# Optimization experiments

Hardware: AMD Instinct MI355X
Metric: run time of the kernel (lower is better)

## Reference

```python
import jax, jax.numpy as jnp
import numpy as np

N = 50000
E = 1600000
IN = 128
HID = 128
OUT = 64
NEG_SLOPE = 0.2  # DGL GATConv default leaky_relu slope


def _gat_layer(h, src, dst, W, al, ar, b, res=None, act=True):
    """DGL GATConv layer on an edge-list graph.
    h: [N, F_in]; W: [F_in, H*D]; al, ar, b: [H, D]; res: None | [N,H,D].
    Returns [N, H, D].
    """
    H, D = al.shape
    f = (h @ W).reshape(N, H, D)                      # fc projection
    el = jnp.sum(f * al, axis=-1)                     # [N, H]
    er = jnp.sum(f * ar, axis=-1)                     # [N, H]
    e = jax.nn.leaky_relu(el[src] + er[dst], NEG_SLOPE)  # [E, H]
    # edge softmax over incoming edges of each dst node
    m = jax.ops.segment_max(e, dst, num_segments=N)   # [N, H]
    ex = jnp.exp(e - m[dst])                          # [E, H]
    s = jax.ops.segment_sum(ex, dst, num_segments=N)  # [N, H]
    alpha = ex / s[dst]                               # [E, H]
    msg = f[src] * alpha[..., None]                   # [E, H, D]
    rst = jax.ops.segment_sum(msg, dst, num_segments=N)  # [N, H, D]
    if res is not None:
        rst = rst + res
    rst = rst + b                                     # bias [H, D] broadcast
    if act:
        rst = jax.nn.elu(rst)
    return rst


def setup_inputs() -> dict:
    key = jax.random.key(0)
    ks = jax.random.split(key, 16)
    x = jax.random.normal(ks[0], (N, IN), dtype=jnp.float32)
    src = jax.random.randint(ks[1], (E,), 0, N)
    dst = jax.random.randint(ks[2], (E,), 0, N)
    sc = 0.05
    # layer 0: IN -> 8 heads x 16, no residual, elu
    W0 = jax.random.normal(ks[3], (IN, 8 * 16), dtype=jnp.float32) * sc
    al0 = jax.random.normal(ks[4], (8, 16), dtype=jnp.float32) * sc
    ar0 = jax.random.normal(ks[5], (8, 16), dtype=jnp.float32) * sc
    b0 = jnp.zeros((8, 16), dtype=jnp.float32)
    # layer 1: HID -> 8 heads x 16, identity residual (HID == 8*16), elu
    W1 = jax.random.normal(ks[6], (HID, 8 * 16), dtype=jnp.float32) * sc
    al1 = jax.random.normal(ks[7], (8, 16), dtype=jnp.float32) * sc
    ar1 = jax.random.normal(ks[8], (8, 16), dtype=jnp.float32) * sc
    b1 = jnp.zeros((8, 16), dtype=jnp.float32)
    # layer 2: HID -> 1 head x 64, linear residual (128 != 64), no act
    W2 = jax.random.normal(ks[9], (HID, 1 * OUT), dtype=jnp.float32) * sc
    al2 = jax.random.normal(ks[10], (1, OUT), dtype=jnp.float32) * sc
    ar2 = jax.random.normal(ks[11], (1, OUT), dtype=jnp.float32) * sc
    b2 = jnp.zeros((1, OUT), dtype=jnp.float32)
    resW2 = jax.random.normal(ks[12], (HID, 1 * OUT), dtype=jnp.float32) * sc
    return {"x": x, "src": src, "dst": dst,
            "W0": W0, "al0": al0, "ar0": ar0, "b0": b0,
            "W1": W1, "al1": al1, "ar1": ar1, "b1": b1,
            "W2": W2, "al2": al2, "ar2": ar2, "b2": b2,
            "resW2": resW2}


def reference(x, src, dst, W0, al0, ar0, b0, W1, al1, ar1, b1,
              W2, al2, ar2, b2, resW2):
    # layer 0: no residual, elu, flatten heads (dropout=0)
    h = _gat_layer(x, src, dst, W0, al0, ar0, b0, res=None, act=True)
    h = h.reshape(N, -1)  # [N, 128]
    # layer 1: identity residual, elu, flatten heads
    res1 = h.reshape(N, 8, 16)
    h = _gat_layer(h, src, dst, W1, al1, ar1, b1, res=res1, act=True)
    h = h.reshape(N, -1)  # [N, 128]
    # layer 2: linear residual, no activation, mean over heads
    res2 = (h @ resW2).reshape(N, 1, OUT)
    h = _gat_layer(h, src, dst, W2, al2, ar2, b2, res=res2, act=False)
    return h.mean(axis=1)  # [N, 64]
```

## Files before the change

kernel.cpp:

```cpp
#include <hip/hip_runtime.h>
#include <hip/hip_fp16.h>
#include <math.h>


#define GN 50000
#define GE 1600000
#define NB 391
#define NBLK_A 512
#define CHUNK 3125

typedef _Float16 half8 __attribute__((ext_vector_type(8)));
typedef _Float16 half4v __attribute__((ext_vector_type(4)));
typedef float f32x4 __attribute__((ext_vector_type(4)));


__global__ __launch_bounds__(256) void bucketA(const int* __restrict__ dst, int* __restrict__ cnt) {
    __shared__ int hist[NB];
    for (int i = threadIdx.x; i < NB; i += 256) hist[i] = 0;
    __syncthreads();
    int b = blockIdx.x;
    int beg = b * CHUNK, end = beg + CHUNK;
    for (int i = beg + threadIdx.x; i < end; i += 256)
        atomicAdd(&hist[dst[i] >> 7], 1);
    __syncthreads();
    for (int k = threadIdx.x; k < NB; k += 256)
        cnt[k * NBLK_A + b] = hist[k];
}

__global__ __launch_bounds__(512) void bucketB(int* __restrict__ cnt, int* __restrict__ tot) {
    __shared__ int s[512];
    int k = blockIdx.x, t = threadIdx.x;
    int* row = cnt + k * NBLK_A;
    s[t] = row[t];
    __syncthreads();
    for (int ofs = 1; ofs < 512; ofs <<= 1) {
        int v = (t >= ofs) ? s[t - ofs] : 0;
        __syncthreads();
        s[t] += v;
        __syncthreads();
    }
    row[t] = (t == 0) ? 0 : s[t - 1];
    if (t == 511) tot[k] = s[511];
}

__global__ __launch_bounds__(512) void bucketB2(const int* __restrict__ tot, int* __restrict__ base,
                                                int* __restrict__ offs) {
    __shared__ int s[512];
    int t = threadIdx.x;
    s[t] = (t < NB) ? tot[t] : 0;
    __syncthreads();
    for (int ofs = 1; ofs < 512; ofs <<= 1) {
        int v = (t >= ofs) ? s[t - ofs] : 0;
        __syncthreads();
        s[t] += v;
        __syncthreads();
    }
    if (t <= NB) base[t] = (t == 0) ? 0 : s[t - 1];
    if (t == 0) offs[GN] = GE;
}

__global__ __launch_bounds__(256) void bucketC(const int* __restrict__ src, const int* __restrict__ dst,
                                               const int* __restrict__ cnt, const int* __restrict__ base,
                                               unsigned* __restrict__ ebuf) {
    __shared__ int cur[NB];
    int b = blockIdx.x;
    for (int k = threadIdx.x; k < NB; k += 256)
        cur[k] = base[k] + cnt[k * NBLK_A + b];
    __syncthreads();
    int beg = b * CHUNK, end = beg + CHUNK;
    for (int i = beg + threadIdx.x; i < end; i += 256) {
        int d = dst[i];
        int pos = atomicAdd(&cur[d >> 7], 1);
        ebuf[pos] = (unsigned)src[i] | ((unsigned)(d & 127) << 16);
    }
}

__global__ __launch_bounds__(256) void bucketD(const unsigned* __restrict__ ebuf, const int* __restrict__ base,
                                               int* __restrict__ offs, int* __restrict__ csrc) {
    __shared__ int hist[4096];
    __shared__ int psum[256];
    int k = blockIdx.x, t = threadIdx.x;
    #pragma unroll
    for (int i = 0; i < 16; ++i) hist[t * 16 + i] = 0;
    __syncthreads();
    int lo = base[k], hi = base[k + 1];
    for (int i = lo + t; i < hi; i += 256) {
        unsigned v = ebuf[i];
        unsigned key = ((v >> 16) << 5) | ((v & 0xFFFFu) >> 11);
        atomicAdd(&hist[key], 1);
    }
    __syncthreads();
    int loc[16];
    int s = 0;
    #pragma unroll
    for (int i = 0; i < 16; ++i) { loc[i] = s; s += hist[t * 16 + i]; }
    psum[t] = s;
    __syncthreads();
    for (int ofs = 1; ofs < 256; ofs <<= 1) {
        int v = (t >= ofs) ? psum[t - ofs] : 0;
        __syncthreads();
        psum[t] += v;
        __syncthreads();
    }
    int basek = lo + ((t == 0) ? 0 : psum[t - 1]);
    #pragma unroll
    for (int i = 0; i < 16; ++i) hist[t * 16 + i] = basek + loc[i];
    __syncthreads();
    if (t < 128) {
        int node = (k << 7) + t;
        if (node < GN) offs[node] = hist[t * 32];
    }
    __syncthreads();
    for (int i = lo + t; i < hi; i += 256) {
        unsigned v = ebuf[i];
        unsigned key = ((v >> 16) << 5) | ((v & 0xFFFFu) >> 11);
        int pos = atomicAdd(&hist[key], 1);
        csrc[pos] = (int)(v & 0xFFFFu);
    }
}


__global__ __launch_bounds__(256) void prep(const float* __restrict__ W0, const float* __restrict__ W1,
                                            const float* __restrict__ W2, const float* __restrict__ rW2,
                                            const float* __restrict__ al0, const float* __restrict__ ar0,
                                            const float* __restrict__ al1, const float* __restrict__ ar1,
                                            const float* __restrict__ al2, const float* __restrict__ ar2,
                                            _Float16* __restrict__ w0t, _Float16* __restrict__ w1t,
                                            _Float16* __restrict__ w2t, _Float16* __restrict__ rw2t,
                                            _Float16* __restrict__ aB0, _Float16* __restrict__ aB1,
                                            _Float16* __restrict__ aB2) {
    int i = blockIdx.x * 256 + threadIdx.x;
    if (i < 16384) {
        int n = i >> 7, k = i & 127;
        w0t[i] = (_Float16)W0[k * 128 + n];
        w1t[i] = (_Float16)W1[k * 128 + n];
    }
    if (i < 8192) {
        int n = i >> 7, k = i & 127;
        w2t[i] = (_Float16)W2[k * 64 + n];
        rw2t[i] = (_Float16)rW2[k * 64 + n];
    }
    if (i < 2048) {
        int n = i >> 7, k = i & 127;
        _Float16 v0 = (_Float16)0.f, v1 = (_Float16)0.f, v2 = (_Float16)0.f;
        if (n < 8) {
            if ((k >> 4) == n) {
                v0 = (_Float16)al0[n * 16 + (k & 15)];
                v1 = (_Float16)al1[n * 16 + (k & 15)];
            }
        } else {
            int h = n - 8;
            if ((k >> 4) == h) {
                v0 = (_Float16)ar0[h * 16 + (k & 15)];
                v1 = (_Float16)ar1[h * 16 + (k & 15)];
            }
        }
        if (n == 0 && k < 64) v2 = (_Float16)al2[k];
        if (n == 1 && k < 64) v2 = (_Float16)ar2[k];
        aB0[i] = v0; aB1[i] = v1; aB2[i] = v2;
    }
}


template <int NT, bool AF32, bool DUAL, bool MULTI>
__global__ __launch_bounds__(256) void gemm_att(const void* __restrict__ Av,
                                                const _Float16* __restrict__ WT,
                                                const _Float16* __restrict__ WT2,
                                                const _Float16* __restrict__ attB,
                                                _Float16* __restrict__ C, _Float16* __restrict__ C2,
                                                float* __restrict__ elb, float* __restrict__ erb,
                                                int nrows) {
    const int N = NT * 16;
    __shared__ _Float16 lt[4][16][NT * 16 + 4];
    int wave = threadIdx.x >> 6, lane = threadIdx.x & 63;
    int quad = lane >> 4, l16 = lane & 15;
    int m = blockIdx.x * 64 + wave * 16 + l16;
    int mc = (m < nrows) ? m : (nrows - 1);
    half8 a[4];
    if (AF32) {
        const float* ap = (const float*)Av + (size_t)mc * 128 + quad * 8;
        #pragma unroll
        for (int kk = 0; kk < 4; ++kk) {
            float4 u = *(const float4*)(ap + kk * 32);
            float4 v = *(const float4*)(ap + kk * 32 + 4);
            half8 t;
            t[0] = (_Float16)u.x; t[1] = (_Float16)u.y; t[2] = (_Float16)u.z; t[3] = (_Float16)u.w;
            t[4] = (_Float16)v.x; t[5] = (_Float16)v.y; t[6] = (_Float16)v.z; t[7] = (_Float16)v.w;
            a[kk] = t;
        }
    } else {
        const _Float16* ap = (const _Float16*)Av + (size_t)mc * 128 + quad * 8;
        #pragma unroll
        for (int kk = 0; kk < 4; ++kk) a[kk] = *(const half8*)(ap + kk * 32);
    }
    f32x4 acc[NT];
    f32x4 acc2[DUAL ? NT : 1];
    #pragma unroll
    for (int nt = 0; nt < NT; ++nt) acc[nt] = (f32x4){0.f, 0.f, 0.f, 0.f};
    if (DUAL) {
        #pragma unroll
        for (int nt = 0; nt < NT; ++nt) acc2[nt] = (f32x4){0.f, 0.f, 0.f, 0.f};
    }
    const _Float16* wp = WT + (size_t)l16 * 128 + quad * 8;
    const _Float16* wp2 = DUAL ? (WT2 + (size_t)l16 * 128 + quad * 8) : WT;
    #pragma unroll
    for (int nt = 0; nt < NT; ++nt) {
        #pragma unroll
        for (int kk = 0; kk < 4; ++kk) {
            half8 b = *(const half8*)(wp + nt * 16 * 128 + kk * 32);
            acc[nt] = __builtin_amdgcn_mfma_f32_16x16x32_f16(a[kk], b, acc[nt], 0, 0, 0);
            if (DUAL) {
                half8 b2 = *(const half8*)(wp2 + nt * 16 * 128 + kk * 32);
                acc2[nt] = __builtin_amdgcn_mfma_f32_16x16x32_f16(a[kk], b2, acc2[nt], 0, 0, 0);
            }
        }
    }
    int row0 = blockIdx.x * 64 + wave * 16 + quad * 4;
    #pragma unroll
    for (int nt = 0; nt < NT; ++nt) {
        #pragma unroll
        for (int r = 0; r < 4; ++r) {
            _Float16 hv = (_Float16)acc[nt][r];
            lt[wave][quad * 4 + r][nt * 16 + l16] = hv;
            int row = row0 + r;
            if (row < nrows) {
                C[(size_t)row * N + nt * 16 + l16] = hv;
                if (DUAL) C2[(size_t)row * N + nt * 16 + l16] = (_Float16)acc2[nt][r];
            }
        }
    }
    f32x4 att = {0.f, 0.f, 0.f, 0.f};
    const _Float16* bp = attB + (size_t)l16 * 128 + quad * 8;
    constexpr int KCH = (NT == 8) ? 4 : 2;
    #pragma unroll
    for (int kk = 0; kk < KCH; ++kk) {
        const _Float16* lp = &lt[wave][l16][kk * 32 + quad * 8];
        half4v lo = *(const half4v*)lp;
        half4v hi = *(const half4v*)(lp + 4);
        half8 af = __builtin_shufflevector(lo, hi, 0, 1, 2, 3, 4, 5, 6, 7);
        half8 bf = *(const half8*)(bp + kk * 32);
        att = __builtin_amdgcn_mfma_f32_16x16x32_f16(af, bf, att, 0, 0, 0);
    }
    if (MULTI) {
        int hh = l16 & 7;
        float* dstp = (l16 < 8) ? elb : erb;
        #pragma unroll
        for (int r = 0; r < 4; ++r) {
            int row = row0 + r;
            if (row < nrows) dstp[row * 8 + hh] = att[r];
        }
    } else {
        if (l16 < 2) {
            float* dstp = (l16 == 0) ? elb : erb;
            #pragma unroll
            for (int r = 0; r < 4; ++r) {
                int row = row0 + r;
                if (row < nrows) dstp[row] = att[r];
            }
        }
    }
}


__global__ __launch_bounds__(256) void agg_multi(const int* __restrict__ offs, const int* __restrict__ csrc,
                                                 const _Float16* __restrict__ fh, const float* __restrict__ el,
                                                 const float* __restrict__ er, const float* __restrict__ bias,
                                                 const _Float16* __restrict__ resid, _Float16* __restrict__ out,
                                                 int n) {
    int node = blockIdx.x * 16 + (threadIdx.x >> 4);
    int lg = threadIdx.x & 15;
    if (node >= n) return;
    int head = lg >> 1;
    float ern = er[node * 8 + head];
    int beg = offs[node], end = offs[node + 1];
    float acc[8] = {};
    float ssum = 0.f;
    int e = beg;
    for (; e + 4 <= end; e += 4) {
        int s0 = csrc[e], s1 = csrc[e + 1], s2 = csrc[e + 2], s3 = csrc[e + 3];
        float e0 = el[s0 * 8 + head] + ern;
        float e1 = el[s1 * 8 + head] + ern;
        float e2 = el[s2 * 8 + head] + ern;
        float e3 = el[s3 * 8 + head] + ern;
        half8 q0 = *(const half8*)(fh + (size_t)s0 * 128 + lg * 8);
        half8 q1 = *(const half8*)(fh + (size_t)s1 * 128 + lg * 8);
        half8 q2 = *(const half8*)(fh + (size_t)s2 * 128 + lg * 8);
        half8 q3 = *(const half8*)(fh + (size_t)s3 * 128 + lg * 8);
        e0 = fmaxf(e0, 0.2f * e0);
        e1 = fmaxf(e1, 0.2f * e1);
        e2 = fmaxf(e2, 0.2f * e2);
        e3 = fmaxf(e3, 0.2f * e3);
        float w0 = __expf(e0), w1 = __expf(e1), w2 = __expf(e2), w3 = __expf(e3);
        ssum += (w0 + w1) + (w2 + w3);
        #pragma unroll
        for (int j = 0; j < 8; ++j)
            acc[j] += w0 * (float)q0[j] + w1 * (float)q1[j]
                    + w2 * (float)q2[j] + w3 * (float)q3[j];
    }
    for (; e < end; ++e) {
        int s = csrc[e];
        float ev = el[s * 8 + head] + ern;
        ev = fmaxf(ev, 0.2f * ev);
        float w = __expf(ev);
        half8 q = *(const half8*)(fh + (size_t)s * 128 + lg * 8);
        ssum += w;
        #pragma unroll
        for (int j = 0; j < 8; ++j) acc[j] += w * (float)q[j];
    }
    float inv = (ssum > 0.f) ? 1.0f / ssum : 0.f;
    float o[8];
    #pragma unroll
    for (int j = 0; j < 8; ++j) o[j] = acc[j] * inv + bias[lg * 8 + j];
    if (resid) {
        half8 r = *(const half8*)(resid + (size_t)node * 128 + lg * 8);
        #pragma unroll
        for (int j = 0; j < 8; ++j) o[j] += (float)r[j];
    }
    half8 ov;
    #pragma unroll
    for (int j = 0; j < 8; ++j) {
        float v = o[j];
        v = (v > 0.f) ? v : expm1f(v);
        ov[j] = (_Float16)v;
    }
    *(half8*)(out + (size_t)node * 128 + lg * 8) = ov;
}

__global__ __launch_bounds__(256) void agg_single(const int* __restrict__ offs, const int* __restrict__ csrc,
                                                  const _Float16* __restrict__ fh, const float* __restrict__ el,
                                                  const float* __restrict__ er, const float* __restrict__ bias,
                                                  const _Float16* __restrict__ resid, float* __restrict__ out,
                                                  int n) {
    int node = blockIdx.x * 16 + (threadIdx.x >> 4);
    int lg = threadIdx.x & 15;
    if (node >= n) return;
    float ern = er[node];
    int beg = offs[node], end = offs[node + 1];
    float acc[4] = {};
    float ssum = 0.f;
    int e = beg;
    for (; e + 4 <= end; e += 4) {
        int s0 = csrc[e], s1 = csrc[e + 1], s2 = csrc[e + 2], s3 = csrc[e + 3];
        float e0 = el[s0] + ern;
        float e1 = el[s1] + ern;
        float e2 = el[s2] + ern;
        float e3 = el[s3] + ern;
        half4v q0 = *(const half4v*)(fh + (size_t)s0 * 64 + lg * 4);
        half4v q1 = *(const half4v*)(fh + (size_t)s1 * 64 + lg * 4);
        half4v q2 = *(const half4v*)(fh + (size_t)s2 * 64 + lg * 4);
        half4v q3 = *(const half4v*)(fh + (size_t)s3 * 64 + lg * 4);
        e0 = fmaxf(e0, 0.2f * e0);
        e1 = fmaxf(e1, 0.2f * e1);
        e2 = fmaxf(e2, 0.2f * e2);
        e3 = fmaxf(e3, 0.2f * e3);
        float w0 = __expf(e0), w1 = __expf(e1), w2 = __expf(e2), w3 = __expf(e3);
        ssum += (w0 + w1) + (w2 + w3);
        #pragma unroll
        for (int j = 0; j < 4; ++j)
            acc[j] += w0 * (float)q0[j] + w1 * (float)q1[j]
                    + w2 * (float)q2[j] + w3 * (float)q3[j];
    }
    for (; e < end; ++e) {
        int s = csrc[e];
        float ev = el[s] + ern;
        ev = fmaxf(ev, 0.2f * ev);
        float w = __expf(ev);
        half4v q = *(const half4v*)(fh + (size_t)s * 64 + lg * 4);
        ssum += w;
        #pragma unroll
        for (int j = 0; j < 4; ++j) acc[j] += w * (float)q[j];
    }
    float inv = (ssum > 0.f) ? 1.0f / ssum : 0.f;
    half4v r = *(const half4v*)(resid + (size_t)node * 64 + lg * 4);
    float4 o;
    o.x = acc[0] * inv + bias[lg * 4 + 0] + (float)r[0];
    o.y = acc[1] * inv + bias[lg * 4 + 1] + (float)r[1];
    o.z = acc[2] * inv + bias[lg * 4 + 2] + (float)r[2];
    o.w = acc[3] * inv + bias[lg * 4 + 3] + (float)r[3];
    *(float4*)(out + (size_t)node * 64 + lg * 4) = o;
}


extern "C" void kernel_launch(void* const* d_in, const int* in_sizes, int n_in,
                              void* d_out, int out_size, void* d_ws, size_t ws_size,
                              hipStream_t stream) {
    const float* x     = (const float*)d_in[0];
    const int*   src   = (const int*)d_in[1];
    const int*   dst   = (const int*)d_in[2];
    const float* W0    = (const float*)d_in[3];
    const float* al0   = (const float*)d_in[4];
    const float* ar0   = (const float*)d_in[5];
    const float* b0    = (const float*)d_in[6];
    const float* W1    = (const float*)d_in[7];
    const float* al1   = (const float*)d_in[8];
    const float* ar1   = (const float*)d_in[9];
    const float* b1    = (const float*)d_in[10];
    const float* W2    = (const float*)d_in[11];
    const float* al2   = (const float*)d_in[12];
    const float* ar2   = (const float*)d_in[13];
    const float* b2    = (const float*)d_in[14];
    const float* resW2 = (const float*)d_in[15];
    float* out = (float*)d_out;

    char* w = (char*)d_ws;
    auto alloc = [&](size_t bytes) {
        char* p = w;
        w += (bytes + 255) & ~(size_t)255;
        return p;
    };
    int*      base  = (int*)alloc((size_t)(NB + 1) * 4);
    int*      offs  = (int*)alloc((size_t)(GN + 1) * 4);
    int*      csrc  = (int*)alloc((size_t)GE * 4);
    _Float16* fbuf  = (_Float16*)alloc((size_t)GN * 128 * 2);
    float*    elb   = (float*)alloc((size_t)GN * 8 * 4);
    float*    erb   = (float*)alloc((size_t)GN * 8 * 4);
    _Float16* hA    = (_Float16*)alloc((size_t)GN * 128 * 2);
    _Float16* hB    = (_Float16*)alloc((size_t)GN * 128 * 2);
    _Float16* res2  = (_Float16*)alloc((size_t)GN * 64 * 2);
    _Float16* w0t   = (_Float16*)alloc(128 * 128 * 2);
    _Float16* w1t   = (_Float16*)alloc(128 * 128 * 2);
    _Float16* w2t   = (_Float16*)alloc(64 * 128 * 2);
    _Float16* rw2t  = (_Float16*)alloc(64 * 128 * 2);
    _Float16* aB0   = (_Float16*)alloc(16 * 128 * 2);
    _Float16* aB1   = (_Float16*)alloc(16 * 128 * 2);
    _Float16* aB2   = (_Float16*)alloc(16 * 128 * 2);

    int*      cnt  = (int*)hA;
    int*      tot  = (int*)hA + NB * NBLK_A;
    unsigned* ebuf = (unsigned*)hB;

    bucketA<<<NBLK_A, 256, 0, stream>>>(dst, cnt);
    bucketB<<<NB, 512, 0, stream>>>(cnt, tot);
    bucketB2<<<1, 512, 0, stream>>>(tot, base, offs);
    bucketC<<<NBLK_A, 256, 0, stream>>>(src, dst, cnt, base, ebuf);
    bucketD<<<NB, 256, 0, stream>>>(ebuf, base, offs, csrc);

    prep<<<64, 256, 0, stream>>>(W0, W1, W2, resW2, al0, ar0, al1, ar1, al2, ar2,
                                 w0t, w1t, w2t, rw2t, aB0, aB1, aB2);

    dim3 gblk(256);
    int gemmGrid = (GN + 63) / 64;
    int aggGrid = (GN + 15) / 16;

    gemm_att<8, true, false, true><<<gemmGrid, gblk, 0, stream>>>(
        x, w0t, nullptr, aB0, fbuf, nullptr, elb, erb, GN);
    agg_multi<<<aggGrid, gblk, 0, stream>>>(offs, csrc, fbuf, elb, erb, b0, nullptr, hA, GN);

    gemm_att<8, false, false, true><<<gemmGrid, gblk, 0, stream>>>(
        hA, w1t, nullptr, aB1, fbuf, nullptr, elb, erb, GN);
    agg_multi<<<aggGrid, gblk, 0, stream>>>(offs, csrc, fbuf, elb, erb, b1, hA, hB, GN);

    gemm_att<4, false, true, false><<<gemmGrid, gblk, 0, stream>>>(
        hB, w2t, rw2t, aB2, fbuf, res2, elb, erb, GN);
    agg_single<<<aggGrid, gblk, 0, stream>>>(offs, csrc, fbuf, elb, erb, b2, res2, out, GN);
}
```

Before: 370.7 us.

## Sort edges by finer source sub-bucket and unroll aggregation gathers by eight

The per-destination-bucket counting sort in bucketD now keys on 128 source sub-ranges per destination node instead of 32, using a 64 KB shared histogram. This orders each node's incoming edges more tightly by source id, which should improve cache locality of the feature gathers. Both aggregation kernels also gain an 8-edge unrolled loop that issues all index, logit and feature loads before doing the math, to keep more memory requests in flight. The larger shared array lowers bucketD occupancy and the wider unroll raises register pressure.

```diff
diff --git a/kernel.cpp b/kernel.cpp
--- a/kernel.cpp
+++ b/kernel.cpp
@@ -77,23 +77,21 @@
 
 __global__ __launch_bounds__(256) void bucketD(const unsigned* __restrict__ ebuf, const int* __restrict__ base,
                                                int* __restrict__ offs, int* __restrict__ csrc) {
-    __shared__ int hist[4096];
+    __shared__ int hist[16384];
     __shared__ int psum[256];
     int k = blockIdx.x, t = threadIdx.x;
-    #pragma unroll
-    for (int i = 0; i < 16; ++i) hist[t * 16 + i] = 0;
+    for (int i = t; i < 16384; i += 256) hist[i] = 0;
     __syncthreads();
     int lo = base[k], hi = base[k + 1];
     for (int i = lo + t; i < hi; i += 256) {
         unsigned v = ebuf[i];
-        unsigned key = ((v >> 16) << 5) | ((v & 0xFFFFu) >> 11);
+        unsigned key = ((v >> 16) << 7) | ((v & 0xFFFFu) >> 9);
         atomicAdd(&hist[key], 1);
     }
     __syncthreads();
-    int loc[16];
     int s = 0;
-    #pragma unroll
-    for (int i = 0; i < 16; ++i) { loc[i] = s; s += hist[t * 16 + i]; }
+    #pragma unroll 8
+    for (int i = 0; i < 64; ++i) s += hist[t * 64 + i];
     psum[t] = s;
     __syncthreads();
     for (int ofs = 1; ofs < 256; ofs <<= 1) {
@@ -102,18 +100,22 @@
         psum[t] += v;
         __syncthreads();
     }
-    int basek = lo + ((t == 0) ? 0 : psum[t - 1]);
-    #pragma unroll
-    for (int i = 0; i < 16; ++i) hist[t * 16 + i] = basek + loc[i];
+    int run = lo + ((t == 0) ? 0 : psum[t - 1]);
+    #pragma unroll 8
+    for (int i = 0; i < 64; ++i) {
+        int c = hist[t * 64 + i];
+        hist[t * 64 + i] = run;
+        run += c;
+    }
     __syncthreads();
     if (t < 128) {
         int node = (k << 7) + t;
-        if (node < GN) offs[node] = hist[t * 32];
+        if (node < GN) offs[node] = hist[t * 128];
     }
     __syncthreads();
     for (int i = lo + t; i < hi; i += 256) {
         unsigned v = ebuf[i];
-        unsigned key = ((v >> 16) << 5) | ((v & 0xFFFFu) >> 11);
+        unsigned key = ((v >> 16) << 7) | ((v & 0xFFFFu) >> 9);
         int pos = atomicAdd(&hist[key], 1);
         csrc[pos] = (int)(v & 0xFFFFu);
     }
@@ -276,6 +278,25 @@
     float acc[8] = {};
     float ssum = 0.f;
     int e = beg;
+    for (; e + 8 <= end; e += 8) {
+        int s_[8];
+        float ee[8];
+        half8 q[8];
+        #pragma unroll
+        for (int j = 0; j < 8; ++j) s_[j] = csrc[e + j];
+        #pragma unroll
+        for (int j = 0; j < 8; ++j) ee[j] = el[s_[j] * 8 + head] + ern;
+        #pragma unroll
+        for (int j = 0; j < 8; ++j) q[j] = *(const half8*)(fh + (size_t)s_[j] * 128 + lg * 8);
+        #pragma unroll
+        for (int j = 0; j < 8; ++j) {
+            float ev = fmaxf(ee[j], 0.2f * ee[j]);
+            float w = __expf(ev);
+            ssum += w;
+            #pragma unroll
+            for (int i = 0; i < 8; ++i) acc[i] += w * (float)q[j][i];
+        }
+    }
     for (; e + 4 <= end; e += 4) {
         int s0 = csrc[e], s1 = csrc[e + 1], s2 = csrc[e + 2], s3 = csrc[e + 3];
         float e0 = el[s0 * 8 + head] + ern;
@@ -293,9 +314,9 @@
         float w0 = __expf(e0), w1 = __expf(e1), w2 = __expf(e2), w3 = __expf(e3);
         ssum += (w0 + w1) + (w2 + w3);
         #pragma unroll
-        for (int j = 0; j < 8; ++j)
-            acc[j] += w0 * (float)q0[j] + w1 * (float)q1[j]
-                    + w2 * (float)q2[j] + w3 * (float)q3[j];
+        for (int i = 0; i < 8; ++i)
+            acc[i] += w0 * (float)q0[i] + w1 * (float)q1[i]
+                    + w2 * (float)q2[i] + w3 * (float)q3[i];
     }
     for (; e < end; ++e) {
         int s = csrc[e];
@@ -305,7 +326,7 @@
         half8 q = *(const half8*)(fh + (size_t)s * 128 + lg * 8);
         ssum += w;
         #pragma unroll
-        for (int j = 0; j < 8; ++j) acc[j] += w * (float)q[j];
+        for (int i = 0; i < 8; ++i) acc[i] += w * (float)q[i];
     }
     float inv = (ssum > 0.f) ? 1.0f / ssum : 0.f;
     float o[8];
@@ -339,6 +360,25 @@
     float acc[4] = {};
     float ssum = 0.f;
     int e = beg;
+    for (; e + 8 <= end; e += 8) {
+        int s_[8];
+        float ee[8];
+        half4v q[8];
+        #pragma unroll
+        for (int j = 0; j < 8; ++j) s_[j] = csrc[e + j];
+        #pragma unroll
+        for (int j = 0; j < 8; ++j) ee[j] = el[s_[j]] + ern;
+        #pragma unroll
+        for (int j = 0; j < 8; ++j) q[j] = *(const half4v*)(fh + (size_t)s_[j] * 64 + lg * 4);
+        #pragma unroll
+        for (int j = 0; j < 8; ++j) {
+            float ev = fmaxf(ee[j], 0.2f * ee[j]);
+            float w = __expf(ev);
+            ssum += w;
+            #pragma unroll
+            for (int i = 0; i < 4; ++i) acc[i] += w * (float)q[j][i];
+        }
+    }
     for (; e + 4 <= end; e += 4) {
         int s0 = csrc[e], s1 = csrc[e + 1], s2 = csrc[e + 2], s3 = csrc[e + 3];
         float e0 = el[s0] + ern;
@@ -356,9 +396,9 @@
         float w0 = __expf(e0), w1 = __expf(e1), w2 = __expf(e2), w3 = __expf(e3);
         ssum += (w0 + w1) + (w2 + w3);
         #pragma unroll
-        for (int j = 0; j < 4; ++j)
-            acc[j] += w0 * (float)q0[j] + w1 * (float)q1[j]
-                    + w2 * (float)q2[j] + w3 * (float)q3[j];
+        for (int i = 0; i < 4; ++i)
+            acc[i] += w0 * (float)q0[i] + w1 * (float)q1[i]
+                    + w2 * (float)q2[i] + w3 * (float)q3[i];
     }
     for (; e < end; ++e) {
         int s = csrc[e];
@@ -368,7 +408,7 @@
         half4v q = *(const half4v*)(fh + (size_t)s * 64 + lg * 4);
         ssum += w;
         #pragma unroll
-        for (int j = 0; j < 4; ++j) acc[j] += w * (float)q[j];
+        for (int i = 0; i < 4; ++i) acc[i] += w * (float)q[i];
     }
     float inv = (ssum > 0.f) ? 1.0f / ssum : 0.f;
     half4v r = *(const half4v*)(resid + (size_t)node * 64 + lg * 4);
```

Result: no change. 373.3 us (+0.7%).

## Sort nodes by in-degree to balance aggregation work across wavefront lanes

Applied to the files above, without the earlier changes.

Adds a counting sort of destination nodes by (clamped) in-degree, built with a histogram, two scan kernels and a scatter, producing a permutation. The aggregation kernels process nodes in this permuted order so node groups within a wavefront have similar edge counts, reducing divergence and tail imbalance. The trade-off is four extra kernel launches, an extra indirection load, and loss of contiguity for per-node reads and writes.

```diff
diff --git a/kernel.cpp b/kernel.cpp
--- a/kernel.cpp
+++ b/kernel.cpp
@@ -8,6 +8,8 @@
 #define NB 391
 #define NBLK_A 512
 #define CHUNK 3125
+#define NBD 200
+#define DCH 250
 
 typedef _Float16 half8 __attribute__((ext_vector_type(8)));
 typedef _Float16 half4v __attribute__((ext_vector_type(4)));
@@ -116,6 +118,67 @@
         unsigned key = ((v >> 16) << 5) | ((v & 0xFFFFu) >> 11);
         int pos = atomicAdd(&hist[key], 1);
         csrc[pos] = (int)(v & 0xFFFFu);
+    }
+}
+
+
+__global__ __launch_bounds__(256) void dhist(const int* __restrict__ offs, int* __restrict__ dcnt) {
+    __shared__ int hist[128];
+    int b = blockIdx.x, t = threadIdx.x;
+    if (t < 128) hist[t] = 0;
+    __syncthreads();
+    int n = b * DCH + t;
+    if (t < DCH && n < GN) {
+        int d = offs[n + 1] - offs[n];
+        d = (d > 127) ? 127 : d;
+        atomicAdd(&hist[d], 1);
+    }
+    __syncthreads();
+    if (t < 128) dcnt[t * NBD + b] = hist[t];
+}
+
+__global__ __launch_bounds__(256) void dscanB(int* __restrict__ dcnt, int* __restrict__ dtot) {
+    __shared__ int s[256];
+    int k = blockIdx.x, t = threadIdx.x;
+    int* row = dcnt + k * NBD;
+    s[t] = (t < NBD) ? row[t] : 0;
+    __syncthreads();
+    for (int ofs = 1; ofs < 256; ofs <<= 1) {
+        int v = (t >= ofs) ? s[t - ofs] : 0;
+        __syncthreads();
+        s[t] += v;
+        __syncthreads();
+    }
+    if (t < NBD) row[t] = (t == 0) ? 0 : s[t - 1];
+    if (t == 255) dtot[k] = s[255];
+}
+
+__global__ __launch_bounds__(128) void dscanB2(const int* __restrict__ dtot, int* __restrict__ dbase) {
+    __shared__ int s[128];
+    int t = threadIdx.x;
+    s[t] = dtot[t];
+    __syncthreads();
+    for (int ofs = 1; ofs < 128; ofs <<= 1) {
+        int v = (t >= ofs) ? s[t - ofs] : 0;
+        __syncthreads();
+        s[t] += v;
+        __syncthreads();
+    }
+    dbase[t] = (t == 0) ? 0 : s[t - 1];
+}
+
+__global__ __launch_bounds__(256) void dscat(const int* __restrict__ offs, const int* __restrict__ dcnt,
+                                             const int* __restrict__ dbase, int* __restrict__ perm) {
+    __shared__ int cur[128];
+    int b = blockIdx.x, t = threadIdx.x;
+    if (t < 128) cur[t] = dbase[t] + dcnt[t * NBD + b];
+    __syncthreads();
+    int n = b * DCH + t;
+    if (t < DCH && n < GN) {
+        int d = offs[n + 1] - offs[n];
+        d = (d > 127) ? 127 : d;
+        int pos = atomicAdd(&cur[d], 1);
+        perm[pos] = n;
     }
 }
 
@@ -263,13 +326,15 @@
 
 
 __global__ __launch_bounds__(256) void agg_multi(const int* __restrict__ offs, const int* __restrict__ csrc,
+                                                 const int* __restrict__ perm,
                                                  const _Float16* __restrict__ fh, const float* __restrict__ el,
                                                  const float* __restrict__ er, const float* __restrict__ bias,
                                                  const _Float16* __restrict__ resid, _Float16* __restrict__ out,
                                                  int n) {
-    int node = blockIdx.x * 16 + (threadIdx.x >> 4);
+    int slot = blockIdx.x * 16 + (threadIdx.x >> 4);
     int lg = threadIdx.x & 15;
-    if (node >= n) return;
+    if (slot >= n) return;
+    int node = perm[slot];
     int head = lg >> 1;
     float ern = er[node * 8 + head];
     int beg = offs[node], end = offs[node + 1];
@@ -293,9 +358,9 @@
         float w0 = __expf(e0), w1 = __expf(e1), w2 = __expf(e2), w3 = __expf(e3);
         ssum += (w0 + w1) + (w2 + w3);
         #pragma unroll
-        for (int j = 0; j < 8; ++j)
-            acc[j] += w0 * (float)q0[j] + w1 * (float)q1[j]
-                    + w2 * (float)q2[j] + w3 * (float)q3[j];
+        for (int i = 0; i < 8; ++i)
+            acc[i] += w0 * (float)q0[i] + w1 * (float)q1[i]
+                    + w2 * (float)q2[i] + w3 * (float)q3[i];
     }
     for (; e < end; ++e) {
         int s = csrc[e];
@@ -305,7 +370,7 @@
         half8 q = *(const half8*)(fh + (size_t)s * 128 + lg * 8);
         ssum += w;
         #pragma unroll
-        for (int j = 0; j < 8; ++j) acc[j] += w * (float)q[j];
+        for (int i = 0; i < 8; ++i) acc[i] += w * (float)q[i];
     }
     float inv = (ssum > 0.f) ? 1.0f / ssum : 0.f;
     float o[8];
@@ -327,13 +392,15 @@
 }
 
 __global__ __launch_bounds__(256) void agg_single(const int* __restrict__ offs, const int* __restrict__ csrc,
+                                                  const int* __restrict__ perm,
                                                   const _Float16* __restrict__ fh, const float* __restrict__ el,
                                                   const float* __restrict__ er, const float* __restrict__ bias,
                                                   const _Float16* __restrict__ resid, float* __restrict__ out,
                                                   int n) {
-    int node = blockIdx.x * 16 + (threadIdx.x >> 4);
+    int slot = blockIdx.x * 16 + (threadIdx.x >> 4);
     int lg = threadIdx.x & 15;
-    if (node >= n) return;
+    if (slot >= n) return;
+    int node = perm[slot];
     float ern = er[node];
     int beg = offs[node], end = offs[node + 1];
     float acc[4] = {};
@@ -356,9 +423,9 @@
         float w0 = __expf(e0), w1 = __expf(e1), w2 = __expf(e2), w3 = __expf(e3);
         ssum += (w0 + w1) + (w2 + w3);
         #pragma unroll
-        for (int j = 0; j < 4; ++j)
-            acc[j] += w0 * (float)q0[j] + w1 * (float)q1[j]
-                    + w2 * (float)q2[j] + w3 * (float)q3[j];
+        for (int i = 0; i < 4; ++i)
+            acc[i] += w0 * (float)q0[i] + w1 * (float)q1[i]
+                    + w2 * (float)q2[i] + w3 * (float)q3[i];
     }
     for (; e < end; ++e) {
         int s = csrc[e];
@@ -368,7 +435,7 @@
         half4v q = *(const half4v*)(fh + (size_t)s * 64 + lg * 4);
         ssum += w;
         #pragma unroll
-        for (int j = 0; j < 4; ++j) acc[j] += w * (float)q[j];
+        for (int i = 0; i < 4; ++i) acc[i] += w * (float)q[i];
     }
     float inv = (ssum > 0.f) ? 1.0f / ssum : 0.f;
     half4v r = *(const half4v*)(resid + (size_t)node * 64 + lg * 4);
@@ -411,6 +478,10 @@
     int*      base  = (int*)alloc((size_t)(NB + 1) * 4);
     int*      offs  = (int*)alloc((size_t)(GN + 1) * 4);
     int*      csrc  = (int*)alloc((size_t)GE * 4);
+    int*      perm  = (int*)alloc((size_t)GN * 4);
+    int*      dcnt  = (int*)alloc((size_t)128 * NBD * 4);
+    int*      dtot  = (int*)alloc(128 * 4);
+    int*      dbase = (int*)alloc(128 * 4);
     _Float16* fbuf  = (_Float16*)alloc((size_t)GN * 128 * 2);
     float*    elb   = (float*)alloc((size_t)GN * 8 * 4);
     float*    erb   = (float*)alloc((size_t)GN * 8 * 4);
@@ -435,6 +506,11 @@
     bucketC<<<NBLK_A, 256, 0, stream>>>(src, dst, cnt, base, ebuf);
     bucketD<<<NB, 256, 0, stream>>>(ebuf, base, offs, csrc);
 
+    dhist<<<NBD, 256, 0, stream>>>(offs, dcnt);
+    dscanB<<<128, 256, 0, stream>>>(dcnt, dtot);
+    dscanB2<<<1, 128, 0, stream>>>(dtot, dbase);
+    dscat<<<NBD, 256, 0, stream>>>(offs, dcnt, dbase, perm);
+
     prep<<<64, 256, 0, stream>>>(W0, W1, W2, resW2, al0, ar0, al1, ar1, al2, ar2,
                                  w0t, w1t, w2t, rw2t, aB0, aB1, aB2);
 
@@ -444,13 +520,13 @@
 
     gemm_att<8, true, false, true><<<gemmGrid, gblk, 0, stream>>>(
         x, w0t, nullptr, aB0, fbuf, nullptr, elb, erb, GN);
-    agg_multi<<<aggGrid, gblk, 0, stream>>>(offs, csrc, fbuf, elb, erb, b0, nullptr, hA, GN);
+    agg_multi<<<aggGrid, gblk, 0, stream>>>(offs, csrc, perm, fbuf, elb, erb, b0, nullptr, hA, GN);
 
     gemm_att<8, false, false, true><<<gemmGrid, gblk, 0, stream>>>(
         hA, w1t, nullptr, aB1, fbuf, nullptr, elb, erb, GN);
-    agg_multi<<<aggGrid, gblk, 0, stream>>>(offs, csrc, fbuf, elb, erb, b1, hA, hB, GN);
+    agg_multi<<<aggGrid, gblk, 0, stream>>>(offs, csrc, perm, fbuf, elb, erb, b1, hA, hB, GN);
 
     gemm_att<4, false, true, false><<<gemmGrid, gblk, 0, stream>>>(
         hB, w2t, rw2t, aB2, fbuf, res2, elb, erb, GN);
-    agg_single<<<aggGrid, gblk, 0, stream>>>(offs, csrc, fbuf, elb, erb, b2, res2, out, GN);
-}
+    agg_single<<<aggGrid, gblk, 0, stream>>>(offs, csrc, perm, fbuf, elb, erb, b2, res2, out, GN);
+}
```

Result: slower. 390.9 us (+5.5%).
